# Performance work log

Hardware: AMD Instinct MI355X
Metric: run time of the kernel (lower is better)

The kernel has to match this reference:

```python
import jax, jax.numpy as jnp
import numpy as np

N, P, S, CORE, H, HEADS, B = 49152, 256, 256, 192, 256, 8, 1
D = H // HEADS  # head_dim = 32
EPS = 1e-5


def setup_inputs() -> dict:
    key = jax.random.key(0)
    ks = jax.random.split(key, 8)
    x = jax.random.normal(ks[0], (B, N, H), dtype=jnp.float32)
    # cores tile all N nodes exactly once (KMeans-like partition), plus random overlap ring
    core = jnp.arange(N, dtype=jnp.int32).reshape(P, CORE)
    ov = jax.random.randint(ks[1], (P, S - CORE), 0, N, dtype=jnp.int32)
    patch_idx = jnp.concatenate([core, ov], axis=1)                      # [P,S]
    core_mask = jnp.concatenate(
        [jnp.ones((P, CORE), bool), jnp.zeros((P, S - CORE), bool)], axis=1)  # [P,S]
    def w(k):
        return jax.random.normal(k, (H, H), dtype=jnp.float32) * 0.02
    return dict(
        x=x, patch_idx=patch_idx, core_mask=core_mask,
        Wq=w(ks[2]), bq=jnp.zeros((H,), jnp.float32),
        Wk=w(ks[3]), bk=jnp.zeros((H,), jnp.float32),
        Wv=w(ks[4]), bv=jnp.zeros((H,), jnp.float32),
        Wo=w(ks[5]), bo=jnp.zeros((H,), jnp.float32),
        ln_g=jnp.ones((H,), jnp.float32), ln_b=jnp.zeros((H,), jnp.float32),
    )


def reference(x, patch_idx, core_mask, Wq, bq, Wk, bk, Wv, bv, Wo, bo, ln_g, ln_b):
    # x: [B,N,H]; patch_idx: [P,S] int; core_mask: [P,S] bool
    px = x[:, patch_idx]                                   # gather -> [B,P,S,H]
    def proj(W, b):
        return (px @ W.T + b).reshape(B, P, S, HEADS, D)
    Q, K, V = proj(Wq, bq), proj(Wk, bk), proj(Wv, bv)
    scores = jnp.einsum('bpihd,bpjhd->bphij', Q, K) / jnp.sqrt(jnp.float32(D))
    attn = jax.nn.softmax(scores, axis=-1)                 # dropout is identity in eval
    att = jnp.einsum('bphij,bpjhd->bpihd', attn, V).reshape(B, P, S, H)
    out = att @ Wo.T + bo                                  # [B,P,S,H]
    # scatter-add only core slots back to nodes, track update counts
    contrib = jnp.where(core_mask[None, :, :, None], out, 0.0).reshape(B, P * S, H)
    flat = patch_idx.reshape(-1)
    acc = jnp.zeros((B, N, H), x.dtype).at[:, flat].add(contrib)
    cnt = jnp.zeros((N,), x.dtype).at[flat].add(core_mask.reshape(-1).astype(x.dtype))
    acc = acc / jnp.clip(cnt, 1.0)[None, :, None]
    # residual + LayerNorm (biased variance, as torch)
    y = x + acc
    mu = jnp.mean(y, axis=-1, keepdims=True)
    var = jnp.var(y, axis=-1, keepdims=True)
    return (y - mu) / jnp.sqrt(var + EPS) * ln_g + ln_b
```

## Files before the change

kernel.cpp:

```cpp
#include <hip/hip_runtime.h>

#define PP 256
#define SS 256
#define CORE_ 192
#define HH 256
#define NHEAD 8
#define DD 32

typedef __attribute__((ext_vector_type(4))) float f32x4;
typedef __attribute__((ext_vector_type(8))) short s8v;
typedef __attribute__((ext_vector_type(4))) short s4v;

__device__ __forceinline__ float bf2f(unsigned short u) {
    union { unsigned int i; float f; } c; c.i = ((unsigned int)u) << 16; return c.f;
}
__device__ __forceinline__ unsigned short f2bf(float f) {
    union { float f; unsigned int i; } c; c.f = f;
    unsigned int i = c.i;
    return (unsigned short)((i + 0x7fffu + ((i >> 16) & 1u)) >> 16);
}

__device__ __forceinline__ void gload16(const unsigned short* g, unsigned short* l) {
    __builtin_amdgcn_global_load_lds(
        (const __attribute__((address_space(1))) void*)g,
        (__attribute__((address_space(3))) void*)l, 16, 0, 0);
}

#define SW(row, chunk) ((chunk) ^ (((row) >> 1) & 3))
__device__ __forceinline__ int swcol(int c, int row) {
    return (c & ~31) | (((((c >> 3) & 3) ^ ((row >> 1) & 3))) << 3) | (c & 7);
}

__global__ __launch_bounds__(256) void k_prep(
    const float* __restrict__ Wq, const float* __restrict__ Wk,
    const float* __restrict__ Wv, const float* __restrict__ Wo,
    const float* __restrict__ bq, const float* __restrict__ bk,
    const float* __restrict__ bv,
    unsigned short* __restrict__ Wb, float* __restrict__ bb) {
    int bid = blockIdx.x, tid = threadIdx.x;
    if (bid >= 128) {
        int which = bid - 128;
        const float* b = which == 0 ? bq : which == 1 ? bk : bv;
        bb[which * 256 + tid] = b[tid];
        return;
    }
    int c = bid * 256 + tid;
    int row = c >> 5;
    int within = c & 31;
    int w = within >> 2, sl = within & 3;
    const float* src = row < 256 ? Wq : row < 512 ? Wk : row < 768 ? Wv : Wo;
    const float* sp = src + (size_t)(row & 255) * 256 + w * 32 + SW(row, sl) * 8;
    float4 a = *(const float4*)sp;
    float4 b4 = *(const float4*)(sp + 4);
    s8v wv;
    wv[0] = (short)f2bf(a.x); wv[1] = (short)f2bf(a.y);
    wv[2] = (short)f2bf(a.z); wv[3] = (short)f2bf(a.w);
    wv[4] = (short)f2bf(b4.x); wv[5] = (short)f2bf(b4.y);
    wv[6] = (short)f2bf(b4.z); wv[7] = (short)f2bf(b4.w);
    *(s8v*)(Wb + (size_t)row * 256 + w * 32 + sl * 8) = wv;
}

__global__ __launch_bounds__(256) void k_qkv(
    const float* __restrict__ x, const int* __restrict__ pidx,
    const unsigned short* __restrict__ Wb, const float* __restrict__ bb,
    unsigned short* __restrict__ qkv) {
    int p = blockIdx.x, mt = blockIdx.y, ng = blockIdx.z;
    if (ng == 0 && mt == 3) return;
    __shared__ unsigned short As[2][64][32];
    __shared__ unsigned short Bs[2][256][32];
    int tid = threadIdx.x;
    int wave = tid >> 6, lane = tid & 63;
    int g = lane >> 4, c0 = lane & 15;
    f32x4 acc[4][4] = {};
    int arow = tid >> 2, aseg = tid & 3;
    int node = pidx[p * SS + mt * 64 + arow];
    const float* asrc = x + (size_t)node * HH + aseg * 8;
    const unsigned short* wsrc = Wb + (size_t)ng * 256 * 256;

    auto stage = [&](int k0, int b) {
#pragma unroll
        for (int j = 0; j < 4; ++j) {
            int chunk = j * 256 + wave * 64 + lane;
            int row = chunk >> 2, c8 = chunk & 3;
            gload16(wsrc + (size_t)row * 256 + k0 + c8 * 8,
                    &Bs[b][0][0] + (size_t)(j * 256 + wave * 64) * 8);
        }
        float4 v0 = *(const float4*)(asrc + k0);
        float4 v1 = *(const float4*)(asrc + k0 + 4);
        s8v aw;
        aw[0] = (short)f2bf(v0.x); aw[1] = (short)f2bf(v0.y);
        aw[2] = (short)f2bf(v0.z); aw[3] = (short)f2bf(v0.w);
        aw[4] = (short)f2bf(v1.x); aw[5] = (short)f2bf(v1.y);
        aw[6] = (short)f2bf(v1.z); aw[7] = (short)f2bf(v1.w);
        *(s8v*)&As[b][arow][SW(arow, aseg) * 8] = aw;
    };

    stage(0, 0);
    __syncthreads();
#pragma unroll
    for (int ks = 0; ks < 8; ++ks) {
        int b = ks & 1;
        if (ks < 7) stage((ks + 1) * 32, b ^ 1);
        s8v af[4], bfv[4];
#pragma unroll
        for (int m2 = 0; m2 < 4; ++m2) {
            int r = m2 * 16 + c0;
            af[m2] = *(const s8v*)&As[b][r][SW(r, g) * 8];
        }
#pragma unroll
        for (int nt = 0; nt < 4; ++nt) {
            int r = wave * 64 + nt * 16 + c0;
            bfv[nt] = *(const s8v*)&Bs[b][r][SW(r, g) * 8];
        }
#pragma unroll
        for (int m2 = 0; m2 < 4; ++m2)
#pragma unroll
            for (int nt = 0; nt < 4; ++nt)
                acc[m2][nt] = __builtin_amdgcn_mfma_f32_16x16x32_bf16(
                    af[m2], bfv[nt], acc[m2][nt], 0, 0, 0);
        __syncthreads();
    }
#pragma unroll
    for (int nt = 0; nt < 4; ++nt) {
        int ncol = wave * 64 + nt * 16 + c0;
        float bv_ = bb[ng * 256 + ncol];
#pragma unroll
        for (int m2 = 0; m2 < 4; ++m2)
#pragma unroll
            for (int r = 0; r < 4; ++r) {
                int srow = mt * 64 + m2 * 16 + g * 4 + r;
                int sc = (ng == 1) ? swcol(ncol, srow) : ncol;
                qkv[((size_t)p * SS + srow) * 768 + ng * 256 + sc] =
                    f2bf(acc[m2][nt][r] + bv_);
            }
    }
}

__global__ __launch_bounds__(256) void k_attn(
    const unsigned short* __restrict__ qkv, unsigned short* __restrict__ att) {
    int p = blockIdx.x, h = blockIdx.y;
    __shared__ unsigned short Ks[256][32];
    __shared__ unsigned short Vt[32][256];
    __shared__ unsigned short Pb[4][16][256];
    int tid = threadIdx.x;
    int wave = tid >> 6, lane = tid & 63;
    int g = lane >> 4, c0 = lane & 15;

#pragma unroll
    for (int j = 0; j < 4; ++j) {
        int chunk = j * 256 + wave * 64 + lane;
        int row = chunk >> 2, c8 = chunk & 3;
        gload16(qkv + ((size_t)p * SS + row) * 768 + 256 + h * DD + c8 * 8,
                &Ks[0][0] + (size_t)(j * 256 + wave * 64) * 8);
    }
    {
        int chunk = tid & 3, rb = tid >> 2;
#pragma unroll
        for (int pass = 0; pass < 4; ++pass) {
            int row = rb + pass * 64;
            s8v vv = *(const s8v*)(qkv + ((size_t)p * SS + row) * 768 + 512 + h * DD + chunk * 8);
            int cj = row >> 3, jo = row & 7;
#pragma unroll
            for (int e = 0; e < 8; ++e) {
                int d = chunk * 8 + e;
                Vt[d][((cj ^ ((d >> 1) & 7)) << 3) + jo] = (unsigned short)vv[e];
            }
        }
    }
    __syncthreads();

    const float scale = 0.17677669529663687f;
    int cs = (c0 >> 1) & 7;

    for (int mi = 0; mi < 3; ++mi) {
        int q0 = (wave * 3 + mi) * 16;
        s8v qa = *(const s8v*)(qkv + ((size_t)p * SS + q0 + c0) * 768 + h * DD + g * 8);
        f32x4 sacc[16];
#pragma unroll
        for (int jt = 0; jt < 16; ++jt) {
            int row = jt * 16 + c0;
            s8v kf = *(const s8v*)&Ks[row][SW(row, g) * 8];
            sacc[jt] = __builtin_amdgcn_mfma_f32_16x16x32_bf16(
                qa, kf, f32x4{0.f, 0.f, 0.f, 0.f}, 0, 0, 0);
        }
        float linv[4];
#pragma unroll
        for (int r = 0; r < 4; ++r) {
            float mx = sacc[0][r];
#pragma unroll
            for (int jt = 1; jt < 16; ++jt) mx = fmaxf(mx, sacc[jt][r]);
#pragma unroll
            for (int off = 1; off < 16; off <<= 1)
                mx = fmaxf(mx, __shfl_xor(mx, off, 64));
            float sum = 0.f;
#pragma unroll
            for (int jt = 0; jt < 16; ++jt) {
                float e = __expf((sacc[jt][r] - mx) * scale);
                sacc[jt][r] = e;
                sum += e;
            }
#pragma unroll
            for (int off = 1; off < 16; off <<= 1)
                sum += __shfl_xor(sum, off, 64);
            linv[r] = 1.f / sum;
            int qq = g * 4 + r;
            int qs = (qq >> 1) & 7;
            unsigned short* prow = &Pb[wave][qq][0];
#pragma unroll
            for (int jt = 0; jt < 16; ++jt) {
                int j0 = jt * 2 + (c0 >> 3);
                prow[((j0 ^ qs) << 3) + (c0 & 7)] = (unsigned short)f2bf(sacc[jt][r]);
            }
        }
        asm volatile("s_waitcnt lgkmcnt(0)" ::: "memory");
        __builtin_amdgcn_sched_barrier(0);
        f32x4 oacc[2] = {f32x4{0.f, 0.f, 0.f, 0.f}, f32x4{0.f, 0.f, 0.f, 0.f}};
#pragma unroll
        for (int kt = 0; kt < 8; ++kt) {
            s8v pa = *(const s8v*)&Pb[wave][c0][(((kt * 4 + g) ^ cs) << 3)];
#pragma unroll
            for (int nt = 0; nt < 2; ++nt) {
                int d = nt * 16 + c0;
                s8v vb = *(const s8v*)&Vt[d][(((kt * 4 + g) ^ ((d >> 1) & 7)) << 3)];
                oacc[nt] = __builtin_amdgcn_mfma_f32_16x16x32_bf16(
                    pa, vb, oacc[nt], 0, 0, 0);
            }
        }
        asm volatile("s_waitcnt lgkmcnt(0)" ::: "memory");
        __builtin_amdgcn_sched_barrier(0);
#pragma unroll
        for (int nt = 0; nt < 2; ++nt)
#pragma unroll
            for (int r = 0; r < 4; ++r) {
                int qq = g * 4 + r;
                int crow = q0 + qq;
                int c = h * DD + nt * 16 + c0;
                att[((size_t)p * CORE_ + crow) * HH + swcol(c, crow)] =
                    f2bf(oacc[nt][r] * linv[r]);
            }
    }
}

__global__ __launch_bounds__(256) void k_out(
    const unsigned short* __restrict__ att, const float* __restrict__ x,
    const unsigned short* __restrict__ Wb, const float* __restrict__ bo,
    const float* __restrict__ ln_g, const float* __restrict__ ln_b,
    float* __restrict__ out) {
    int p = blockIdx.x, mb = blockIdx.y;
    __shared__ unsigned short As[2][64][32];
    __shared__ unsigned short Bs[2][256][32];
    int tid = threadIdx.x;
    int wave = tid >> 6, lane = tid & 63;
    int g = lane >> 4, c0 = lane & 15;
    f32x4 acc[16] = {};

    auto stage = [&](int k0, int b) {
        {
            int chunk = wave * 64 + lane;
            int row = chunk >> 2, c8 = chunk & 3;
            gload16(att + ((size_t)p * CORE_ + mb * 64 + row) * HH + k0 + c8 * 8,
                    &As[b][0][0] + (size_t)(wave * 64) * 8);
        }
#pragma unroll
        for (int j = 0; j < 4; ++j) {
            int chunk = j * 256 + wave * 64 + lane;
            int row = chunk >> 2, c8 = chunk & 3;
            gload16(Wb + (size_t)(768 + row) * 256 + k0 + c8 * 8,
                    &Bs[b][0][0] + (size_t)(j * 256 + wave * 64) * 8);
        }
    };

    stage(0, 0);
    __syncthreads();
#pragma unroll
    for (int ks = 0; ks < 8; ++ks) {
        int b = ks & 1;
        if (ks < 7) stage((ks + 1) * 32, b ^ 1);
        int ar = wave * 16 + c0;
        s8v af = *(const s8v*)&As[b][ar][SW(ar, g) * 8];
#pragma unroll
        for (int nt = 0; nt < 16; ++nt) {
            int r = nt * 16 + c0;
            s8v bfv = *(const s8v*)&Bs[b][r][SW(r, g) * 8];
            acc[nt] = __builtin_amdgcn_mfma_f32_16x16x32_bf16(af, bfv, acc[nt], 0, 0, 0);
        }
        __syncthreads();
    }
    int srow0 = mb * 64 + wave * 16 + g * 4;
    float sum[4] = {0, 0, 0, 0}, ssq[4] = {0, 0, 0, 0};
#pragma unroll
    for (int nt = 0; nt < 16; ++nt) {
        int col = nt * 16 + c0;
        float bov = bo[col];
#pragma unroll
        for (int r = 0; r < 4; ++r) {
            size_t node = (size_t)p * CORE_ + srow0 + r;
            float v = acc[nt][r] + bov + x[node * HH + col];
            acc[nt][r] = v;
            sum[r] += v; ssq[r] += v * v;
        }
    }
#pragma unroll
    for (int off = 1; off < 16; off <<= 1) {
#pragma unroll
        for (int r = 0; r < 4; ++r) {
            sum[r] += __shfl_xor(sum[r], off, 64);
            ssq[r] += __shfl_xor(ssq[r], off, 64);
        }
    }
#pragma unroll
    for (int r = 0; r < 4; ++r) {
        float mu = sum[r] * (1.f / HH);
        float var = ssq[r] * (1.f / HH) - mu * mu;
        float rstd = rsqrtf(var + 1e-5f);
        size_t node = (size_t)p * CORE_ + srow0 + r;
#pragma unroll
        for (int nt = 0; nt < 16; ++nt) {
            int col = nt * 16 + c0;
            out[node * HH + col] = (acc[nt][r] - mu) * rstd * ln_g[col] + ln_b[col];
        }
    }
}

extern "C" void kernel_launch(void* const* d_in, const int* in_sizes, int n_in,
                              void* d_out, int out_size, void* d_ws, size_t ws_size,
                              hipStream_t stream) {
    const float* x   = (const float*)d_in[0];
    const int* pidx  = (const int*)d_in[1];
    const float* Wq  = (const float*)d_in[3];
    const float* bq  = (const float*)d_in[4];
    const float* Wk  = (const float*)d_in[5];
    const float* bk  = (const float*)d_in[6];
    const float* Wv  = (const float*)d_in[7];
    const float* bv  = (const float*)d_in[8];
    const float* Wo  = (const float*)d_in[9];
    const float* bo  = (const float*)d_in[10];
    const float* lng = (const float*)d_in[11];
    const float* lnb = (const float*)d_in[12];

    unsigned short* qkv = (unsigned short*)d_ws;
    unsigned short* att = qkv + (size_t)PP * SS * 768;
    unsigned short* Wb  = att + (size_t)PP * CORE_ * HH;
    float* bb = (float*)(Wb + 1024 * 256);

    k_prep<<<131, 256, 0, stream>>>(Wq, Wk, Wv, Wo, bq, bk, bv, Wb, bb);
    k_qkv<<<dim3(PP, 4, 3), 256, 0, stream>>>(x, pidx, Wb, bb, qkv);
    k_attn<<<dim3(PP, NHEAD), 256, 0, stream>>>(qkv, att);
    k_out<<<dim3(PP, 3), 256, 0, stream>>>(att, x, Wb, bo, lng, lnb, (float*)d_out);
}
```

Measured before the change: 159.3 us.

## Cut LDS footprint in QKV and attention kernels and reorder the QKV grid

The QKV GEMM drops LDS double buffering. It prefetches the next x slice into registers instead, and reorders the grid so that the 12 tiles of one patch launch next to each other, which should help cache reuse of gathered rows. The attention kernel halves its P buffer by writing and consuming the probabilities in two halves. It also loads V with a 4-row transpose that writes 8-byte vectors, restructures the softmax so the four rows are processed together for more ILP, and uses exp2f with a folded scale. The aim is to raise occupancy and cut instruction and LDS-store overhead. The cost is that the single-buffered GEMM can no longer overlap loads with MFMA through LDS, and the two-phase PV path adds extra waits.

```diff
diff --git a/kernel.cpp b/kernel.cpp
--- a/kernel.cpp
+++ b/kernel.cpp
@@ -64,10 +64,11 @@
     const float* __restrict__ x, const int* __restrict__ pidx,
     const unsigned short* __restrict__ Wb, const float* __restrict__ bb,
     unsigned short* __restrict__ qkv) {
-    int p = blockIdx.x, mt = blockIdx.y, ng = blockIdx.z;
+    int bx = blockIdx.x, p = blockIdx.y;
+    int mt = bx / 3, ng = bx % 3;
     if (ng == 0 && mt == 3) return;
-    __shared__ unsigned short As[2][64][32];
-    __shared__ unsigned short Bs[2][256][32];
+    __shared__ unsigned short As[64][32];
+    __shared__ unsigned short Bs[256][32];
     int tid = threadIdx.x;
     int wave = tid >> 6, lane = tid & 63;
     int g = lane >> 4, c0 = lane & 15;
@@ -77,40 +78,39 @@
     const float* asrc = x + (size_t)node * HH + aseg * 8;
     const unsigned short* wsrc = Wb + (size_t)ng * 256 * 256;
 
-    auto stage = [&](int k0, int b) {
+    float4 v0 = *(const float4*)(asrc);
+    float4 v1 = *(const float4*)(asrc + 4);
+#pragma unroll
+    for (int ks = 0; ks < 8; ++ks) {
+        int k0 = ks * 32;
 #pragma unroll
         for (int j = 0; j < 4; ++j) {
             int chunk = j * 256 + wave * 64 + lane;
             int row = chunk >> 2, c8 = chunk & 3;
             gload16(wsrc + (size_t)row * 256 + k0 + c8 * 8,
-                    &Bs[b][0][0] + (size_t)(j * 256 + wave * 64) * 8);
-        }
-        float4 v0 = *(const float4*)(asrc + k0);
-        float4 v1 = *(const float4*)(asrc + k0 + 4);
+                    &Bs[0][0] + (size_t)(j * 256 + wave * 64) * 8);
+        }
         s8v aw;
         aw[0] = (short)f2bf(v0.x); aw[1] = (short)f2bf(v0.y);
         aw[2] = (short)f2bf(v0.z); aw[3] = (short)f2bf(v0.w);
         aw[4] = (short)f2bf(v1.x); aw[5] = (short)f2bf(v1.y);
         aw[6] = (short)f2bf(v1.z); aw[7] = (short)f2bf(v1.w);
-        *(s8v*)&As[b][arow][SW(arow, aseg) * 8] = aw;
-    };
-
-    stage(0, 0);
-    __syncthreads();
-#pragma unroll
-    for (int ks = 0; ks < 8; ++ks) {
-        int b = ks & 1;
-        if (ks < 7) stage((ks + 1) * 32, b ^ 1);
+        *(s8v*)&As[arow][SW(arow, aseg) * 8] = aw;
+        if (ks < 7) {
+            v0 = *(const float4*)(asrc + k0 + 32);
+            v1 = *(const float4*)(asrc + k0 + 36);
+        }
+        __syncthreads();
         s8v af[4], bfv[4];
 #pragma unroll
         for (int m2 = 0; m2 < 4; ++m2) {
             int r = m2 * 16 + c0;
-            af[m2] = *(const s8v*)&As[b][r][SW(r, g) * 8];
+            af[m2] = *(const s8v*)&As[r][SW(r, g) * 8];
         }
 #pragma unroll
         for (int nt = 0; nt < 4; ++nt) {
             int r = wave * 64 + nt * 16 + c0;
-            bfv[nt] = *(const s8v*)&Bs[b][r][SW(r, g) * 8];
+            bfv[nt] = *(const s8v*)&Bs[r][SW(r, g) * 8];
         }
 #pragma unroll
         for (int m2 = 0; m2 < 4; ++m2)
@@ -141,7 +141,7 @@
     int p = blockIdx.x, h = blockIdx.y;
     __shared__ unsigned short Ks[256][32];
     __shared__ unsigned short Vt[32][256];
-    __shared__ unsigned short Pb[4][16][256];
+    __shared__ unsigned short Pb[4][16][128];
     int tid = threadIdx.x;
     int wave = tid >> 6, lane = tid & 63;
     int g = lane >> 4, c0 = lane & 15;
@@ -154,22 +154,26 @@
                 &Ks[0][0] + (size_t)(j * 256 + wave * 64) * 8);
     }
     {
-        int chunk = tid & 3, rb = tid >> 2;
-#pragma unroll
-        for (int pass = 0; pass < 4; ++pass) {
-            int row = rb + pass * 64;
-            s8v vv = *(const s8v*)(qkv + ((size_t)p * SS + row) * 768 + 512 + h * DD + chunk * 8);
-            int cj = row >> 3, jo = row & 7;
-#pragma unroll
-            for (int e = 0; e < 8; ++e) {
-                int d = chunk * 8 + e;
-                Vt[d][((cj ^ ((d >> 1) & 7)) << 3) + jo] = (unsigned short)vv[e];
-            }
+        int dw = tid & 3, jb = tid >> 2;
+        int j0 = jb * 4;
+        const unsigned short* vbase =
+            qkv + ((size_t)p * SS + j0) * 768 + 512 + h * DD + dw * 8;
+        s8v r0 = *(const s8v*)(vbase);
+        s8v r1 = *(const s8v*)(vbase + 768);
+        s8v r2 = *(const s8v*)(vbase + 1536);
+        s8v r3 = *(const s8v*)(vbase + 2304);
+        int cj = j0 >> 3, jo = j0 & 7;
+#pragma unroll
+        for (int e = 0; e < 8; ++e) {
+            int d = dw * 8 + e;
+            s4v w4;
+            w4[0] = r0[e]; w4[1] = r1[e]; w4[2] = r2[e]; w4[3] = r3[e];
+            *(s4v*)&Vt[d][((cj ^ ((d >> 1) & 7)) << 3) + jo] = w4;
         }
     }
     __syncthreads();
 
-    const float scale = 0.17677669529663687f;
+    const float C2 = 0.2550348792930095f;
     int cs = (c0 >> 1) & 7;
 
     for (int mi = 0; mi < 3; ++mi) {
@@ -183,51 +187,67 @@
             sacc[jt] = __builtin_amdgcn_mfma_f32_16x16x32_bf16(
                 qa, kf, f32x4{0.f, 0.f, 0.f, 0.f}, 0, 0, 0);
         }
-        float linv[4];
-#pragma unroll
-        for (int r = 0; r < 4; ++r) {
-            float mx = sacc[0][r];
-#pragma unroll
-            for (int jt = 1; jt < 16; ++jt) mx = fmaxf(mx, sacc[jt][r]);
-#pragma unroll
-            for (int off = 1; off < 16; off <<= 1)
-                mx = fmaxf(mx, __shfl_xor(mx, off, 64));
-            float sum = 0.f;
-#pragma unroll
-            for (int jt = 0; jt < 16; ++jt) {
-                float e = __expf((sacc[jt][r] - mx) * scale);
+        float mx[4], sum[4], linv[4];
+#pragma unroll
+        for (int r = 0; r < 4; ++r) mx[r] = sacc[0][r];
+#pragma unroll
+        for (int jt = 1; jt < 16; ++jt)
+#pragma unroll
+            for (int r = 0; r < 4; ++r) mx[r] = fmaxf(mx[r], sacc[jt][r]);
+#pragma unroll
+        for (int off = 1; off < 16; off <<= 1)
+#pragma unroll
+            for (int r = 0; r < 4; ++r)
+                mx[r] = fmaxf(mx[r], __shfl_xor(mx[r], off, 64));
+#pragma unroll
+        for (int r = 0; r < 4; ++r) sum[r] = 0.f;
+#pragma unroll
+        for (int jt = 0; jt < 16; ++jt)
+#pragma unroll
+            for (int r = 0; r < 4; ++r) {
+                float e = exp2f((sacc[jt][r] - mx[r]) * C2);
                 sacc[jt][r] = e;
-                sum += e;
-            }
-#pragma unroll
-            for (int off = 1; off < 16; off <<= 1)
-                sum += __shfl_xor(sum, off, 64);
-            linv[r] = 1.f / sum;
-            int qq = g * 4 + r;
-            int qs = (qq >> 1) & 7;
-            unsigned short* prow = &Pb[wave][qq][0];
-#pragma unroll
-            for (int jt = 0; jt < 16; ++jt) {
-                int j0 = jt * 2 + (c0 >> 3);
-                prow[((j0 ^ qs) << 3) + (c0 & 7)] = (unsigned short)f2bf(sacc[jt][r]);
-            }
-        }
-        asm volatile("s_waitcnt lgkmcnt(0)" ::: "memory");
-        __builtin_amdgcn_sched_barrier(0);
+                sum[r] += e;
+            }
+#pragma unroll
+        for (int off = 1; off < 16; off <<= 1)
+#pragma unroll
+            for (int r = 0; r < 4; ++r)
+                sum[r] += __shfl_xor(sum[r], off, 64);
+#pragma unroll
+        for (int r = 0; r < 4; ++r) linv[r] = 1.f / sum[r];
+
         f32x4 oacc[2] = {f32x4{0.f, 0.f, 0.f, 0.f}, f32x4{0.f, 0.f, 0.f, 0.f}};
 #pragma unroll
-        for (int kt = 0; kt < 8; ++kt) {
-            s8v pa = *(const s8v*)&Pb[wave][c0][(((kt * 4 + g) ^ cs) << 3)];
-#pragma unroll
-            for (int nt = 0; nt < 2; ++nt) {
-                int d = nt * 16 + c0;
-                s8v vb = *(const s8v*)&Vt[d][(((kt * 4 + g) ^ ((d >> 1) & 7)) << 3)];
-                oacc[nt] = __builtin_amdgcn_mfma_f32_16x16x32_bf16(
-                    pa, vb, oacc[nt], 0, 0, 0);
-            }
-        }
-        asm volatile("s_waitcnt lgkmcnt(0)" ::: "memory");
-        __builtin_amdgcn_sched_barrier(0);
+        for (int half = 0; half < 2; ++half) {
+#pragma unroll
+            for (int r = 0; r < 4; ++r) {
+                int qq = g * 4 + r, qs = (qq >> 1) & 7;
+                unsigned short* prow = &Pb[wave][qq][0];
+#pragma unroll
+                for (int jt = 0; jt < 8; ++jt) {
+                    int j0 = jt * 2 + (c0 >> 3);
+                    prow[((j0 ^ qs) << 3) + (c0 & 7)] =
+                        (unsigned short)f2bf(sacc[half * 8 + jt][r]);
+                }
+            }
+            asm volatile("s_waitcnt lgkmcnt(0)" ::: "memory");
+            __builtin_amdgcn_sched_barrier(0);
+#pragma unroll
+            for (int kt = 0; kt < 4; ++kt) {
+                int ktg = half * 4 + kt;
+                s8v pa = *(const s8v*)&Pb[wave][c0][(((kt * 4 + g) ^ cs) << 3)];
+#pragma unroll
+                for (int nt = 0; nt < 2; ++nt) {
+                    int d = nt * 16 + c0;
+                    s8v vb = *(const s8v*)&Vt[d][(((ktg * 4 + g) ^ ((d >> 1) & 7)) << 3)];
+                    oacc[nt] = __builtin_amdgcn_mfma_f32_16x16x32_bf16(
+                        pa, vb, oacc[nt], 0, 0, 0);
+                }
+            }
+            asm volatile("s_waitcnt lgkmcnt(0)" ::: "memory");
+            __builtin_amdgcn_sched_barrier(0);
+        }
 #pragma unroll
         for (int nt = 0; nt < 2; ++nt)
 #pragma unroll
@@ -344,7 +364,7 @@
     float* bb = (float*)(Wb + 1024 * 256);
 
     k_prep<<<131, 256, 0, stream>>>(Wq, Wk, Wv, Wo, bq, bk, bv, Wb, bb);
-    k_qkv<<<dim3(PP, 4, 3), 256, 0, stream>>>(x, pidx, Wb, bb, qkv);
+    k_qkv<<<dim3(12, PP), 256, 0, stream>>>(x, pidx, Wb, bb, qkv);
     k_attn<<<dim3(PP, NHEAD), 256, 0, stream>>>(qkv, att);
     k_out<<<dim3(PP, 3), 256, 0, stream>>>(att, x, Wb, bo, lng, lnb, (float*)d_out);
 }
```

Measured after the change: 162.5 us. 1.02x slower.
